# Kernel optimization log

Measured on AMD Instinct MI355X. Metric: run time of the kernel, lower is better.

Reference implementation:

```python
import jax, jax.numpy as jnp
import numpy as np

B, C, H, W = 8, 192, 128, 128
NUM_HEADS = 4
EPS = 1e-12  # torch F.normalize default eps
DN = ('NCHW', 'OIHW', 'NCHW')


def setup_inputs() -> dict:
    key = jax.random.key(0)
    k1, k2, k3, k4 = jax.random.split(key, 4)
    x = jax.random.normal(k1, (B, C, H, W), dtype=jnp.float32)
    qkv_w = jax.random.normal(k2, (3 * C, C, 1, 1), dtype=jnp.float32) * 0.05
    dw_w = jax.random.normal(k3, (3 * C, 1, 3, 3), dtype=jnp.float32) * 0.1
    proj_w = jax.random.normal(k4, (C, C, 1, 1), dtype=jnp.float32) * 0.05
    temperature = jnp.ones((NUM_HEADS, 1, 1), dtype=jnp.float32)
    return {"x": x, "qkv_w": qkv_w, "dw_w": dw_w, "proj_w": proj_w,
            "temperature": temperature}


def _l2norm(t):
    # F.normalize(t, dim=-1): divide by max(||t||, eps)
    n = jnp.sqrt(jnp.sum(t * t, axis=-1, keepdims=True))
    return t / jnp.maximum(n, EPS)


def reference(x, qkv_w, dw_w, proj_w, temperature):
    b, c, h, w = x.shape
    nh = NUM_HEADS
    cph = c // nh
    # 1x1 conv -> depthwise 3x3 conv (groups = 3*dim)
    qkv = jax.lax.conv_general_dilated(x, qkv_w, (1, 1), 'VALID',
                                       dimension_numbers=DN)
    qkv = jax.lax.conv_general_dilated(qkv, dw_w, (1, 1), [(1, 1), (1, 1)],
                                       dimension_numbers=DN,
                                       feature_group_count=3 * c)
    q, k, v = jnp.split(qkv, 3, axis=1)
    # [b, nh, cph, h*w]
    q = q.reshape(b, nh, cph, h * w)
    k = k.reshape(b, nh, cph, h * w)
    v = v.reshape(b, nh, cph, h * w)
    q = _l2norm(q)
    k = _l2norm(k)
    # channel attention: [b, nh, cph, cph]
    attn = jnp.einsum('bhcn,bhdn->bhcd', q, k) * temperature
    attn = jax.nn.softmax(attn, axis=-1)
    out = jnp.einsum('bhcd,bhdn->bhcn', attn, v)
    out = out.reshape(b, c, h, w)
    return jax.lax.conv_general_dilated(out, proj_w, (1, 1), 'VALID',
                                        dimension_numbers=DN)
```

## Files before the change

kernel.cpp:

```cpp
#include <hip/hip_runtime.h>
#include <hip/hip_bf16.h>

typedef __hip_bfloat16 bf16;
typedef __attribute__((ext_vector_type(8))) __bf16 bf16x8;
typedef __attribute__((ext_vector_type(4))) float f32x4;
typedef unsigned int u32;

#define HW 16384

static __device__ __forceinline__ float b2f(bf16 v) { return __bfloat162float(v); }
static __device__ __forceinline__ bf16 f2b(float v) { return __float2bfloat16(v); }
static __device__ __forceinline__ float blo(unsigned int w) {
    return __uint_as_float(w << 16);
}
static __device__ __forceinline__ float bhi(unsigned int w) {
    return __uint_as_float(w & 0xffff0000u);
}
static __device__ __forceinline__ unsigned short f2bu(float v) {
    union { bf16 b; unsigned short u; } c; c.b = f2b(v); return c.u;
}

static __device__ __forceinline__ void stf(float* p, float v) { *p = v; }
static __device__ __forceinline__ void stf(bf16* p, float v)  { *p = f2b(v); }

static __device__ __forceinline__ void gload_lds16(const void* g, void* l) {
    __builtin_amdgcn_global_load_lds(
        (const __attribute__((address_space(1))) void*)g,
        (__attribute__((address_space(3))) void*)l, 16, 0, 0);
}

static __device__ __forceinline__ void load8(const float* p, float* v) {
    const float4* q = (const float4*)p;
    float4 a = q[0], b = q[1];
    v[0] = a.x; v[1] = a.y; v[2] = a.z; v[3] = a.w;
    v[4] = b.x; v[5] = b.y; v[6] = b.z; v[7] = b.w;
}
static __device__ __forceinline__ void load8(const bf16* p, float* v) {
    uint4 u = *(const uint4*)p;
    v[0] = blo(u.x); v[1] = bhi(u.x); v[2] = blo(u.y); v[3] = bhi(u.y);
    v[4] = blo(u.z); v[5] = bhi(u.z); v[6] = blo(u.w); v[7] = bhi(u.w);
}

__global__ __launch_bounds__(256) void tr_cast(
    const float* __restrict__ x, bf16* __restrict__ xT)
{
    const int b  = blockIdx.x >> 8;
    const int t  = blockIdx.x & 255;
    const int hw0 = t << 6;
    const float* xb = x + (size_t)b * 192 * HW;

    __shared__ unsigned short T[64][200];

    const int tid = threadIdx.x;
    for (int i = tid; i < 192 * 16; i += 256) {
        int c = i >> 4, seg = i & 15;
        float4 f = *(const float4*)(xb + (size_t)c * HW + hw0 + seg * 4);
        T[seg * 4 + 0][c] = f2bu(f.x);
        T[seg * 4 + 1][c] = f2bu(f.y);
        T[seg * 4 + 2][c] = f2bu(f.z);
        T[seg * 4 + 3][c] = f2bu(f.w);
    }
    __syncthreads();

    const int hw = tid >> 2, c0 = (tid & 3) * 48;
    const uint4* src = (const uint4*)&T[hw][c0];
    uint4* dst = (uint4*)(xT + ((size_t)(b * HW) + hw0 + hw) * 192 + c0);
#pragma unroll
    for (int j = 0; j < 6; j++) dst[j] = src[j];
}

__global__ __launch_bounds__(256) void wcast(
    const float* __restrict__ w, bf16* __restrict__ o, int n4)
{
    int i = blockIdx.x * 256 + threadIdx.x;
    if (i < n4) {
        float4 f = ((const float4*)w)[i];
        u32 lo = (u32)f2bu(f.x) | ((u32)f2bu(f.y) << 16);
        u32 hi = (u32)f2bu(f.z) | ((u32)f2bu(f.w) << 16);
        ((uint2*)o)[i] = make_uint2(lo, hi);
    }
}

template <typename TY>
__global__ __launch_bounds__(256) void gemm_mfma(
    const bf16* __restrict__ Wb, const bf16* __restrict__ Bx,
    TY* __restrict__ Y, int MB)
{
    constexpr int N = HW;
    const int b    = blockIdx.x & 7;
    const int slot = blockIdx.x >> 3;
    const int mb   = slot % MB;
    const int ng   = slot / MB;
    const int m0   = mb * 64;
    const int n0   = ng * 128;

    const char* Bpanel = (const char*)(Bx + (size_t)b * N * 192) + (size_t)n0 * 384;
    TY* Yb = Y + (size_t)b * (MB * 64) * N;

    __shared__ __align__(16) char Bs[49152];

    const int tid  = threadIdx.x;
    const int lane = tid & 63, wave = tid >> 6;
    const int wm = (wave & 1) * 32, wn = (wave >> 1) * 64;
    const int r16 = lane & 15, quad = lane >> 4;

#pragma unroll
    for (int r = 0; r < 12; r++) {
        int L   = r * 4096 + tid * 16;
        int row = L / 384;
        int col = L - row * 384;
        int scol = col ^ ((row & 7) << 4);
        gload_lds16(Bpanel + (size_t)row * 384 + scol,
                    Bs + r * 4096 + wave * 1024);
    }

    const bf16* aBase = Wb + (size_t)(m0 + wm + r16) * 192 + quad * 8;
    bf16x8 aReg[6][2];
#pragma unroll
    for (int ks = 0; ks < 6; ks++)
#pragma unroll
        for (int h = 0; h < 2; h++)
            aReg[ks][h] = *(const bf16x8*)(aBase + h * 16 * 192 + ks * 32);

    asm volatile("s_waitcnt vmcnt(0)" ::: "memory");
    __syncthreads();

    f32x4 acc[2][4];
#pragma unroll
    for (int i = 0; i < 2; i++)
#pragma unroll
        for (int j = 0; j < 4; j++) acc[i][j] = (f32x4){0.f, 0.f, 0.f, 0.f};

    int rbase[4], rxor[4];
#pragma unroll
    for (int sn = 0; sn < 4; sn++) {
        int nl = wn + sn * 16 + r16;
        rbase[sn] = nl * 384;
        rxor[sn]  = (nl & 7) << 4;
    }

#pragma unroll
    for (int ks = 0; ks < 6; ks++) {
#pragma unroll
        for (int sn = 0; sn < 4; sn++) {
            bf16x8 bb = *(const bf16x8*)(
                Bs + rbase[sn] + ((ks * 64 + quad * 16) ^ rxor[sn]));
            acc[0][sn] = __builtin_amdgcn_mfma_f32_16x16x32_bf16(
                aReg[ks][0], bb, acc[0][sn], 0, 0, 0);
            acc[1][sn] = __builtin_amdgcn_mfma_f32_16x16x32_bf16(
                aReg[ks][1], bb, acc[1][sn], 0, 0, 0);
        }
    }

#pragma unroll
    for (int sm = 0; sm < 2; sm++)
#pragma unroll
        for (int sn = 0; sn < 4; sn++) {
            const int gr = m0 + wm + sm * 16 + quad * 4;
            const int gc = n0 + wn + sn * 16 + r16;
#pragma unroll
            for (int r = 0; r < 4; r++)
                stf(Yb + (size_t)(gr + r) * N + gc, acc[sm][sn][r]);
        }
}

__global__ __launch_bounds__(256) void dwconv3x3(
    const bf16* __restrict__ in, const float* __restrict__ wdw,
    bf16* __restrict__ out)
{
    const int plane = blockIdx.x >> 2;
    const int ybase = (blockIdx.x & 3) << 5;
    const int c = plane % 576;
    const bf16* ip = in + ((size_t)plane << 14);

    __shared__ unsigned short Ls[34][128];

    for (int i = threadIdx.x; i < 34 * 16; i += 256) {
        int r = i >> 4, cx = i & 15;
        int y = ybase - 1 + r;
        uint4 v = make_uint4(0u, 0u, 0u, 0u);
        if (y >= 0 && y < 128) v = ((const uint4*)(ip + ((size_t)y << 7)))[cx];
        ((uint4*)Ls[r])[cx] = v;
    }

    float w[9];
#pragma unroll
    for (int i = 0; i < 9; i++) w[i] = wdw[c * 9 + i];

    __syncthreads();

    const int lr = threadIdx.x >> 3;
    const int c0 = (threadIdx.x & 7) << 4;

    float row[3][18];
#pragma unroll
    for (int r3 = 0; r3 < 3; r3++) {
        int rr = lr + r3;
        row[r3][0]  = c0 ? __uint_as_float((unsigned int)Ls[rr][c0 - 1] << 16) : 0.f;
        row[r3][17] = (c0 + 16 < 128) ? __uint_as_float((unsigned int)Ls[rr][c0 + 16] << 16) : 0.f;
        const uint4* rp = (const uint4*)&Ls[rr][c0];
        uint4 p0 = rp[0], p1 = rp[1];
        row[r3][1] = blo(p0.x); row[r3][2] = bhi(p0.x);
        row[r3][3] = blo(p0.y); row[r3][4] = bhi(p0.y);
        row[r3][5] = blo(p0.z); row[r3][6] = bhi(p0.z);
        row[r3][7] = blo(p0.w); row[r3][8] = bhi(p0.w);
        row[r3][9]  = blo(p1.x); row[r3][10] = bhi(p1.x);
        row[r3][11] = blo(p1.y); row[r3][12] = bhi(p1.y);
        row[r3][13] = blo(p1.z); row[r3][14] = bhi(p1.z);
        row[r3][15] = blo(p1.w); row[r3][16] = bhi(p1.w);
    }

    union { unsigned short s[16]; uint4 v[2]; } o;
#pragma unroll
    for (int j = 0; j < 16; j++) {
        float s = 0.f;
#pragma unroll
        for (int r3 = 0; r3 < 3; r3++)
            s += w[r3 * 3 + 0] * row[r3][j] + w[r3 * 3 + 1] * row[r3][j + 1]
               + w[r3 * 3 + 2] * row[r3][j + 2];
        o.s[j] = f2bu(s);
    }
    uint4* op = (uint4*)(out + ((size_t)plane << 14) + ((size_t)(ybase + lr) << 7) + c0);
    op[0] = o.v[0];
    op[1] = o.v[1];
}

__global__ __launch_bounds__(256) void rownorm(
    const bf16* __restrict__ qkv, float* __restrict__ rn)
{
    int r = blockIdx.x;
    int which = (r >= 1536) ? 1 : 0;
    int rr = r - which * 1536;
    int b = rr / 192, c = rr % 192;
    const bf16* p = qkv + ((size_t)(b * 576 + which * 192 + c) << 14);

    float s = 0.f;
    for (int i = threadIdx.x * 8; i < HW; i += 256 * 8) {
        float v[8];
        load8(p + i, v);
#pragma unroll
        for (int j = 0; j < 8; j++) s += v[j] * v[j];
    }
#pragma unroll
    for (int off = 32; off; off >>= 1) s += __shfl_down(s, off);
    __shared__ float red[4];
    if ((threadIdx.x & 63) == 0) red[threadIdx.x >> 6] = s;
    __syncthreads();
    if (threadIdx.x == 0) {
        float t = red[0] + red[1] + red[2] + red[3];
        rn[r] = 1.0f / fmaxf(sqrtf(t), 1e-12f);
    }
}

__global__ __launch_bounds__(256) void attn_dots(
    const bf16* __restrict__ qkv, float* __restrict__ attn)
{
    const int bh = blockIdx.y, b = bh >> 2, h = bh & 3;
    const int n0 = blockIdx.x * 1024;
    const bf16* q  = qkv + ((size_t)(b * 576 + h * 48) << 14);
    const bf16* kp = qkv + ((size_t)(b * 576 + 192 + h * 48) << 14);

    __shared__ float qt[48][68];
    __shared__ float kt[48][68];

    const int tid = threadIdx.x;
    const int cg = tid >> 4, dg = tid & 15;

    float acc[3][3] = {{0.f, 0.f, 0.f}, {0.f, 0.f, 0.f}, {0.f, 0.f, 0.f}};

    for (int s0 = 0; s0 < 1024; s0 += 64) {
        for (int i = tid; i < 48 * 8; i += 256) {
            int rowi = i / 8, cx = (i & 7) * 8;
            size_t off = ((size_t)rowi << 14) + n0 + s0 + cx;
            float v[8];
            load8(q + off, v);
#pragma unroll
            for (int j = 0; j < 8; j++) qt[rowi][cx + j] = v[j];
            load8(kp + off, v);
#pragma unroll
            for (int j = 0; j < 8; j++) kt[rowi][cx + j] = v[j];
        }
        __syncthreads();
#pragma unroll 8
        for (int n = 0; n < 64; n++) {
            float a0 = qt[cg * 3 + 0][n], a1 = qt[cg * 3 + 1][n], a2 = qt[cg * 3 + 2][n];
            float b0 = kt[dg * 3 + 0][n], b1 = kt[dg * 3 + 1][n], b2 = kt[dg * 3 + 2][n];
            acc[0][0] += a0 * b0; acc[0][1] += a0 * b1; acc[0][2] += a0 * b2;
            acc[1][0] += a1 * b0; acc[1][1] += a1 * b1; acc[1][2] += a1 * b2;
            acc[2][0] += a2 * b0; acc[2][1] += a2 * b1; acc[2][2] += a2 * b2;
        }
        __syncthreads();
    }
#pragma unroll
    for (int i = 0; i < 3; i++)
#pragma unroll
        for (int j = 0; j < 3; j++)
            atomicAdd(&attn[(size_t)bh * 2304 + (cg * 3 + i) * 48 + dg * 3 + j],
                      acc[i][j]);
}

__global__ __launch_bounds__(64) void softmax48(
    float* __restrict__ attn, const float* __restrict__ rn,
    const float* __restrict__ temp)
{
    int bh = blockIdx.x, b = bh >> 2, h = bh & 3;
    int c = threadIdx.x;
    if (c >= 48) return;
    float t = temp[h];
    float iq = rn[b * 192 + h * 48 + c];
    const float* ik = rn + 1536 + b * 192 + h * 48;
    float* row = attn + (size_t)bh * 2304 + c * 48;

    float v[48];
    float mx = -1e30f;
#pragma unroll
    for (int d = 0; d < 48; d++) {
        v[d] = row[d] * iq * ik[d] * t;
        mx = fmaxf(mx, v[d]);
    }
    float s = 0.f;
#pragma unroll
    for (int d = 0; d < 48; d++) {
        v[d] = expf(v[d] - mx);
        s += v[d];
    }
    float inv = 1.0f / s;
#pragma unroll
    for (int d = 0; d < 48; d++) row[d] = v[d] * inv;
}

__global__ __launch_bounds__(256) void attn_v_t(
    const float* __restrict__ attn, const bf16* __restrict__ qkv,
    bf16* __restrict__ outT)
{
    const int b = blockIdx.y;
    const int n = blockIdx.x * 256 + threadIdx.x;

    __shared__ float A4[4][2304];
    for (int i = threadIdx.x; i < 4 * 2304; i += 256)
        ((float*)A4)[i] = attn[(size_t)b * 4 * 2304 + i];
    __syncthreads();

    bf16* o = outT + ((size_t)(b * HW) + n) * 192;
#pragma unroll 1
    for (int h = 0; h < 4; h++) {
        const bf16* v = qkv + ((size_t)(b * 576 + 384 + h * 48) << 14) + n;
        float acc[48];
#pragma unroll
        for (int c = 0; c < 48; c++) acc[c] = 0.f;
        for (int d = 0; d < 48; d++) {
            float vd = b2f(v[(size_t)d << 14]);
#pragma unroll
            for (int c = 0; c < 48; c++) acc[c] += A4[h][c * 48 + d] * vd;
        }
        uint4 pk[6];
        u32* pw = (u32*)pk;
#pragma unroll
        for (int j = 0; j < 24; j++)
            pw[j] = (u32)f2bu(acc[2 * j]) | ((u32)f2bu(acc[2 * j + 1]) << 16);
        uint4* d4 = (uint4*)(o + h * 48);
#pragma unroll
        for (int j = 0; j < 6; j++) d4[j] = pk[j];
    }
}

extern "C" void kernel_launch(void* const* d_in, const int* in_sizes, int n_in,
                              void* d_out, int out_size, void* d_ws, size_t ws_size,
                              hipStream_t stream)
{
    const float* x      = (const float*)d_in[0];
    const float* qkv_w  = (const float*)d_in[1];
    const float* dw_w   = (const float*)d_in[2];
    const float* proj_w = (const float*)d_in[3];
    const float* temp   = (const float*)d_in[4];
    float* out = (float*)d_out;

    char* ws = (char*)d_ws;
    const size_t qkvBytes = (size_t)8 * 576 * HW * sizeof(bf16);
    bf16*  qkv0 = (bf16*)ws;
    bf16*  qkv1 = (bf16*)(ws + qkvBytes);
    float* attn = (float*)(ws + 2 * qkvBytes);
    float* rn   = (float*)(ws + 2 * qkvBytes + (size_t)32 * 2304 * sizeof(float));

    bf16* xT    = (bf16*)qkv1;
    bf16* aoutT = (bf16*)qkv0;
    bf16* Wb    = (bf16*)attn;
    bf16* Pb    = (bf16*)(ws + 100 * 1024 * 1024);

    tr_cast<<<dim3(8 * 256), 256, 0, stream>>>(x, xT);
    wcast<<<dim3(108), 256, 0, stream>>>(qkv_w, Wb, 27648);
    gemm_mfma<bf16><<<dim3(8 * 9 * 128), 256, 0, stream>>>(Wb, xT, qkv0, 9);
    dwconv3x3<<<dim3(8 * 576 * 4), 256, 0, stream>>>(qkv0, dw_w, qkv1);
    wcast<<<dim3(36), 256, 0, stream>>>(proj_w, Pb, 9216);
    rownorm<<<dim3(3072), 256, 0, stream>>>(qkv1, rn);
    hipMemsetAsync(attn, 0, (size_t)32 * 2304 * sizeof(float), stream);
    attn_dots<<<dim3(16, 32), 256, 0, stream>>>(qkv1, attn);
    softmax48<<<dim3(32), 64, 0, stream>>>(attn, rn, temp);
    attn_v_t<<<dim3(64, 8), 256, 0, stream>>>(attn, qkv1, aoutT);
    gemm_mfma<float><<<dim3(8 * 3 * 128), 256, 0, stream>>>(Pb, aoutT, out, 3);
}
```

Measured before the change: 573.7 us.

## Split attn-V kernel per head and stage V tile in LDS via direct loads

The attention-times-V kernel now launches one block per (batch, head, 256-column tile) instead of looping over all four heads inside a block, which gives four times as many blocks. Each block copies its 48x256 V tile into shared memory with direct global-to-LDS loads, and each thread keeps its 48 V values in registers. The attention matrix is read straight from global memory with uniform addresses instead of being staged in shared memory. This aims to raise occupancy and parallelism and to make the V loads coalesced. In exchange it relies on scalar or cached reads of the attention matrix and holds more registers per thread.

```diff
diff --git a/kernel.cpp b/kernel.cpp
--- a/kernel.cpp
+++ b/kernel.cpp
@@ -333,35 +333,54 @@
     const float* __restrict__ attn, const bf16* __restrict__ qkv,
     bf16* __restrict__ outT)
 {
-    const int b = blockIdx.y;
-    const int n = blockIdx.x * 256 + threadIdx.x;
-
-    __shared__ float A4[4][2304];
-    for (int i = threadIdx.x; i < 4 * 2304; i += 256)
-        ((float*)A4)[i] = attn[(size_t)b * 4 * 2304 + i];
+    const int nb = blockIdx.x;
+    const int h  = blockIdx.y & 3;
+    const int b  = blockIdx.y >> 2;
+    const int n0 = nb * 256;
+
+    __shared__ __align__(16) char Vs[48 * 512];
+
+    const int tid = threadIdx.x;
+    const int wave = tid >> 6, lane = tid & 63;
+
+    const bf16* vbase = qkv + ((size_t)(b * 576 + 384 + h * 48) << 14) + n0;
+    {
+        const int r0 = wave * 12;
+#pragma unroll
+        for (int i = 0; i < 6; i++) {
+            int r = r0 + i * 2 + (lane >> 5);
+            gload_lds16((const char*)(vbase + ((size_t)r << 14)) + (lane & 31) * 16,
+                        Vs + (size_t)(r0 + i * 2) * 512);
+        }
+    }
+    asm volatile("s_waitcnt vmcnt(0)" ::: "memory");
     __syncthreads();
 
-    bf16* o = outT + ((size_t)(b * HW) + n) * 192;
-#pragma unroll 1
-    for (int h = 0; h < 4; h++) {
-        const bf16* v = qkv + ((size_t)(b * 576 + 384 + h * 48) << 14) + n;
-        float acc[48];
-#pragma unroll
-        for (int c = 0; c < 48; c++) acc[c] = 0.f;
-        for (int d = 0; d < 48; d++) {
-            float vd = b2f(v[(size_t)d << 14]);
-#pragma unroll
-            for (int c = 0; c < 48; c++) acc[c] += A4[h][c * 48 + d] * vd;
-        }
-        uint4 pk[6];
-        u32* pw = (u32*)pk;
-#pragma unroll
-        for (int j = 0; j < 24; j++)
-            pw[j] = (u32)f2bu(acc[2 * j]) | ((u32)f2bu(acc[2 * j + 1]) << 16);
-        uint4* d4 = (uint4*)(o + h * 48);
-#pragma unroll
-        for (int j = 0; j < 6; j++) d4[j] = pk[j];
-    }
+    float v[48];
+#pragma unroll
+    for (int d = 0; d < 48; d++)
+        v[d] = blo((u32)*(const unsigned short*)(Vs + d * 512 + tid * 2));
+
+    const float* __restrict__ Ah = attn + (size_t)(b * 4 + h) * 2304;
+
+    float acc[48];
+#pragma unroll
+    for (int c = 0; c < 48; c++) {
+        float s = 0.f;
+#pragma unroll
+        for (int d = 0; d < 48; d++) s += Ah[c * 48 + d] * v[d];
+        acc[c] = s;
+    }
+
+    bf16* o = outT + ((size_t)(b * HW) + n0 + tid) * 192 + h * 48;
+    uint4 pk[6];
+    u32* pw = (u32*)pk;
+#pragma unroll
+    for (int j = 0; j < 24; j++)
+        pw[j] = (u32)f2bu(acc[2 * j]) | ((u32)f2bu(acc[2 * j + 1]) << 16);
+    uint4* d4 = (uint4*)o;
+#pragma unroll
+    for (int j = 0; j < 6; j++) d4[j] = pk[j];
 }
 
 extern "C" void kernel_launch(void* const* d_in, const int* in_sizes, int n_in,
@@ -396,6 +415,6 @@
     hipMemsetAsync(attn, 0, (size_t)32 * 2304 * sizeof(float), stream);
     attn_dots<<<dim3(16, 32), 256, 0, stream>>>(qkv1, attn);
     softmax48<<<dim3(32), 64, 0, stream>>>(attn, rn, temp);
-    attn_v_t<<<dim3(64, 8), 256, 0, stream>>>(attn, qkv1, aoutT);
+    attn_v_t<<<dim3(64, 32), 256, 0, stream>>>(attn, qkv1, aoutT);
     gemm_mfma<float><<<dim3(8 * 3 * 128), 256, 0, stream>>>(Pb, aoutT, out, 3);
 }
```

New measurement: 537.6 us. 1.07x faster.

## Fold attention matrix into projection weights and run one batched GEMM on V

Applied to the files above, without the earlier changes.

Precomputes a per-batch matrix M = proj_w·blockdiag(attn) in a small kernel, so attn@V and the output projection collapse into a single MFMA GEMM over transposed V. This replaces the scalar attn_v_t kernel, which did 48x48 FMAs per pixel per head with strided V loads. It adds a V transpose pass through LDS, and the GEMM now reads a per-batch weight matrix selected by a new stride argument. Rounding M to bf16 changes numerics slightly.

```diff
diff --git a/kernel.cpp b/kernel.cpp
--- a/kernel.cpp
+++ b/kernel.cpp
@@ -84,7 +84,7 @@
 template <typename TY>
 __global__ __launch_bounds__(256) void gemm_mfma(
     const bf16* __restrict__ Wb, const bf16* __restrict__ Bx,
-    TY* __restrict__ Y, int MB)
+    TY* __restrict__ Y, int MB, int wstride)
 {
     constexpr int N = HW;
     const int b    = blockIdx.x & 7;
@@ -114,7 +114,8 @@
                     Bs + r * 4096 + wave * 1024);
     }
 
-    const bf16* aBase = Wb + (size_t)(m0 + wm + r16) * 192 + quad * 8;
+    const bf16* aBase = Wb + (size_t)b * wstride
+                      + (size_t)(m0 + wm + r16) * 192 + quad * 8;
     bf16x8 aReg[6][2];
 #pragma unroll
     for (int ks = 0; ks < 6; ks++)
@@ -225,6 +226,33 @@
     op[1] = o.v[1];
 }
 
+__global__ __launch_bounds__(256) void vtrans(
+    const bf16* __restrict__ qkv, bf16* __restrict__ vT)
+{
+    const int b  = blockIdx.x >> 8;
+    const int t  = blockIdx.x & 255;
+    const int hw0 = t << 6;
+    const bf16* vb = qkv + ((size_t)(b * 576 + 384) << 14);
+
+    __shared__ unsigned short T[64][200];
+
+    const int tid = threadIdx.x;
+    for (int i = tid; i < 192 * 8; i += 256) {
+        int c = i >> 3, ch = i & 7;
+        uint4 u = *(const uint4*)(vb + ((size_t)c << 14) + hw0 + ch * 8);
+        const unsigned short* us = (const unsigned short*)&u;
+#pragma unroll
+        for (int j = 0; j < 8; j++) T[ch * 8 + j][c] = us[j];
+    }
+    __syncthreads();
+
+    const int hw = tid >> 2, c0 = (tid & 3) * 48;
+    const uint4* src = (const uint4*)&T[hw][c0];
+    uint4* dst = (uint4*)(vT + ((size_t)(b * HW) + hw0 + hw) * 192 + c0);
+#pragma unroll
+    for (int j = 0; j < 6; j++) dst[j] = src[j];
+}
+
 __global__ __launch_bounds__(256) void rownorm(
     const bf16* __restrict__ qkv, float* __restrict__ rn)
 {
@@ -329,39 +357,40 @@
     for (int d = 0; d < 48; d++) row[d] = v[d] * inv;
 }
 
-__global__ __launch_bounds__(256) void attn_v_t(
-    const float* __restrict__ attn, const bf16* __restrict__ qkv,
-    bf16* __restrict__ outT)
-{
-    const int b = blockIdx.y;
-    const int n = blockIdx.x * 256 + threadIdx.x;
-
-    __shared__ float A4[4][2304];
-    for (int i = threadIdx.x; i < 4 * 2304; i += 256)
-        ((float*)A4)[i] = attn[(size_t)b * 4 * 2304 + i];
-    __syncthreads();
-
-    bf16* o = outT + ((size_t)(b * HW) + n) * 192;
-#pragma unroll 1
-    for (int h = 0; h < 4; h++) {
-        const bf16* v = qkv + ((size_t)(b * 576 + 384 + h * 48) << 14) + n;
-        float acc[48];
-#pragma unroll
-        for (int c = 0; c < 48; c++) acc[c] = 0.f;
-        for (int d = 0; d < 48; d++) {
-            float vd = b2f(v[(size_t)d << 14]);
-#pragma unroll
-            for (int c = 0; c < 48; c++) acc[c] += A4[h][c * 48 + d] * vd;
-        }
-        uint4 pk[6];
-        u32* pw = (u32*)pk;
-#pragma unroll
-        for (int j = 0; j < 24; j++)
-            pw[j] = (u32)f2bu(acc[2 * j]) | ((u32)f2bu(acc[2 * j + 1]) << 16);
-        uint4* d4 = (uint4*)(o + h * 48);
-#pragma unroll
-        for (int j = 0; j < 6; j++) d4[j] = pk[j];
-    }
+__global__ __launch_bounds__(192) void pwa(
+    const float* __restrict__ pw, const float* __restrict__ attn,
+    bf16* __restrict__ Mb)
+{
+    const int bh = blockIdx.x, b = bh >> 2, h = bh & 3;
+    __shared__ float As[48 * 48];
+    for (int i = threadIdx.x; i < 2304; i += 192)
+        As[i] = attn[(size_t)bh * 2304 + i];
+    __syncthreads();
+
+    const int i = threadIdx.x;
+    float p[48];
+    const float* pr = pw + (size_t)i * 192 + h * 48;
+#pragma unroll
+    for (int j = 0; j < 12; j++) {
+        float4 f = ((const float4*)pr)[j];
+        p[4 * j] = f.x; p[4 * j + 1] = f.y; p[4 * j + 2] = f.z; p[4 * j + 3] = f.w;
+    }
+    float m[48];
+#pragma unroll
+    for (int d = 0; d < 48; d++) m[d] = 0.f;
+#pragma unroll 4
+    for (int c = 0; c < 48; c++) {
+        float pc = p[c];
+#pragma unroll
+        for (int d = 0; d < 48; d++) m[d] += pc * As[c * 48 + d];
+    }
+    u32 pk[24];
+#pragma unroll
+    for (int j = 0; j < 24; j++)
+        pk[j] = (u32)f2bu(m[2 * j]) | ((u32)f2bu(m[2 * j + 1]) << 16);
+    uint4* o = (uint4*)(Mb + ((size_t)(b * 192) + i) * 192 + h * 48);
+#pragma unroll
+    for (int j = 0; j < 6; j++) o[j] = ((const uint4*)pk)[j];
 }
 
 extern "C" void kernel_launch(void* const* d_in, const int* in_sizes, int n_in,
@@ -382,20 +411,21 @@
     float* attn = (float*)(ws + 2 * qkvBytes);
     float* rn   = (float*)(ws + 2 * qkvBytes + (size_t)32 * 2304 * sizeof(float));
 
-    bf16* xT    = (bf16*)qkv1;
-    bf16* aoutT = (bf16*)qkv0;
-    bf16* Wb    = (bf16*)attn;
-    bf16* Pb    = (bf16*)(ws + 100 * 1024 * 1024);
+    bf16* xT = (bf16*)qkv1;
+    bf16* vT = (bf16*)ws;
+    bf16* Mb = (bf16*)(ws + 104 * 1024 * 1024);
+    bf16* Wb = (bf16*)attn;
 
     tr_cast<<<dim3(8 * 256), 256, 0, stream>>>(x, xT);
     wcast<<<dim3(108), 256, 0, stream>>>(qkv_w, Wb, 27648);
-    gemm_mfma<bf16><<<dim3(8 * 9 * 128), 256, 0, stream>>>(Wb, xT, qkv0, 9);
+    gemm_mfma<bf16><<<dim3(8 * 9 * 128), 256, 0, stream>>>(Wb, xT, qkv0, 9, 0);
     dwconv3x3<<<dim3(8 * 576 * 4), 256, 0, stream>>>(qkv0, dw_w, qkv1);
-    wcast<<<dim3(36), 256, 0, stream>>>(proj_w, Pb, 9216);
+    vtrans<<<dim3(8 * 256), 256, 0, stream>>>(qkv1, vT);
     rownorm<<<dim3(3072), 256, 0, stream>>>(qkv1, rn);
     hipMemsetAsync(attn, 0, (size_t)32 * 2304 * sizeof(float), stream);
     attn_dots<<<dim3(16, 32), 256, 0, stream>>>(qkv1, attn);
     softmax48<<<dim3(32), 64, 0, stream>>>(attn, rn, temp);
-    attn_v_t<<<dim3(64, 8), 256, 0, stream>>>(attn, qkv1, aoutT);
-    gemm_mfma<float><<<dim3(8 * 3 * 128), 256, 0, stream>>>(Pb, aoutT, out, 3);
-}
+    pwa<<<dim3(32), 192, 0, stream>>>(proj_w, attn, Mb);
+    gemm_mfma<float><<<dim3(8 * 3 * 128), 256, 0, stream>>>(
+        Mb, vT, out, 3, 192 * 192);
+}
```

After: 505.0 us. 1.14x faster.
